# Optimization experiments

Hardware: AMD Instinct MI355X
Metric: run time of the kernel (lower is better)

Reference implementation:

```python
import jax, jax.numpy as jnp
import numpy as np

B, S, D = 4, 2048, 1024

def setup_inputs() -> dict:
    key = jax.random.key(0)
    kv, kk, kq, kw = jax.random.split(key, 4)
    scale = 1.0 / np.sqrt(D)
    v = jax.random.normal(kv, (B, S, D), dtype=jnp.float32)
    k = jax.random.normal(kk, (B, S, D), dtype=jnp.float32)
    q = jax.random.normal(kq, (B, S, D), dtype=jnp.float32)
    wi = jax.random.normal(kw, (D, D), dtype=jnp.float32) * scale
    mask = jnp.tril(jnp.ones((S, S), dtype=bool))[None, :, :]  # causal [1,S,S]
    return {"v": v, "k": k, "q": q, "wi": wi, "mask": mask}

def reference(v, k, q, wi, mask):
    # project q, k, v with the shared weight wi
    q = q @ wi
    k = k @ wi
    v = v @ wi
    # scaled dot-product scores [B,S,S]
    scores = jnp.einsum('bqd,bkd->bqk', q, k) / jnp.sqrt(jnp.asarray(q.shape[-1], q.dtype))
    scores = jnp.where(mask, scores, jnp.asarray(-1e10, scores.dtype))
    attn = jax.nn.softmax(scores, axis=-1)
    # residual: q + attn @ v
    return q + jnp.einsum('bqk,bkd->bqd', attn, v)
```

## Files before the change

### kernel.cpp

```cpp
#include <hip/hip_runtime.h>
#include <hip/hip_bf16.h>

typedef __hip_bfloat16 bf16;
typedef short bf16x8 __attribute__((ext_vector_type(8)));
typedef float f32x4 __attribute__((ext_vector_type(4)));

#define HT 16384

__device__ __forceinline__ void gload16(const void* g, void* l) {
    __builtin_amdgcn_global_load_lds(
        (const __attribute__((address_space(1))) void*)g,
        (__attribute__((address_space(3))) void*)l, 16, 0, 0);
}

__device__ __forceinline__ void stage_half(char* lds, const bf16* src, int ld,
                                           int rowbase, int k0, int slotIdx,
                                           int tid)
{
    char* dst = lds + (size_t)slotIdx * HT + tid * 16;
    const int sub = tid >> 3;
    const int cb  = ((tid & 7) ^ (sub & 7)) << 4;
    #pragma unroll
    for (int p = 0; p < 2; ++p) {
        const int row = p * 64 + sub;
        const char* g = (const char*)(src + (size_t)(rowbase + row) * ld + k0) + cb;
        gload16(g, dst + p * 8192);
    }
}

__device__ __forceinline__ bf16x8 ldsfrag(const char* lds, int slotIdx,
                                          int row, int ks, int cb0)
{
    return *(const bf16x8*)(lds + (size_t)slotIdx * HT
                            + row * 128 + (cb0 ^ (ks << 6)));
}

__device__ __forceinline__ float bf2f(short s) {
    union { float f; unsigned u; } c;
    c.u = ((unsigned)(unsigned short)s) << 16;
    return c.f;
}

__launch_bounds__(512, 2)
__global__ void proj_deep(const bf16* __restrict__ A, const bf16* __restrict__ B,
                          bf16* __restrict__ C)
{
    extern __shared__ char lds[];
    const int orig = blockIdx.y * 8 + blockIdx.x;
    const int wk2 = (orig & 7) * 96 + (orig >> 3);
    const int bi = wk2 >> 3, bj = wk2 & 7;
    const int brow = bi * 256, bcol = bj * 128;

    const int tid  = threadIdx.x;
    const int lane = tid & 63;
    const int w    = tid >> 6;
    const int wm   = w >> 1, wn = w & 1;
    const int fr   = lane & 15, fq = lane >> 4;
    const int cb0  = ((fr & 7) ^ fq) << 4;
    const int hA    = wm >> 1;
    const int rA    = (wm & 1) * 64;
    const int rB    = wn * 64;
    const int NT    = 16;

    f32x4 acc[4][4] = {};
    bf16x8 af[4][2], bv[4][2];

    stage_half(lds, A, 1024, brow,       0, 0, tid);
    stage_half(lds, A, 1024, brow + 128, 0, 1, tid);
    stage_half(lds, B, 1024, bcol,       0, 6, tid);
    stage_half(lds, A, 1024, brow,      64, 2, tid);
    stage_half(lds, A, 1024, brow + 128,64, 3, tid);
    stage_half(lds, B, 1024, bcol,     64, 7, tid);
    stage_half(lds, B, 1024, bcol,    128, 8, tid);
    asm volatile("s_waitcnt vmcnt(8)" ::: "memory");
    __builtin_amdgcn_s_barrier();

#define QUAD2(m0, n0)                                                         \
    _Pragma("unroll") for (int dm = 0; dm < 2; ++dm)                          \
    _Pragma("unroll") for (int dn = 0; dn < 2; ++dn)                          \
    _Pragma("unroll") for (int ks = 0; ks < 2; ++ks)                          \
        acc[(m0)+dm][(n0)+dn] = __builtin_amdgcn_mfma_f32_16x16x32_bf16(      \
            af[(m0)+dm][ks], bv[(n0)+dn][ks], acc[(m0)+dm][(n0)+dn], 0, 0, 0);

    for (int t = 0; t < NT; ++t) {
        const int ab  = t % 3;
        const int bb  = 6 + ab;
        const int ab2 = ((t + 2) % 3) * 2;
        const int kA  = min(t + 2, NT - 1) << 6;
        const int kB  = min(t + 3, NT - 1) << 6;
        const int slotA = ab * 2 + hA;

        #pragma unroll
        for (int m = 0; m < 2; ++m)
            #pragma unroll
            for (int ks = 0; ks < 2; ++ks)
                af[m][ks] = ldsfrag(lds, slotA, rA + m * 16 + fr, ks, cb0);
        #pragma unroll
        for (int n = 0; n < 2; ++n)
            #pragma unroll
            for (int ks = 0; ks < 2; ++ks)
                bv[n][ks] = ldsfrag(lds, bb, rB + n * 16 + fr, ks, cb0);
        stage_half(lds, A, 1024, brow, kA, ab2, tid);
        __builtin_amdgcn_s_barrier();
        __builtin_amdgcn_s_setprio(1);
        QUAD2(0, 0)
        __builtin_amdgcn_s_setprio(0);
        __builtin_amdgcn_s_barrier();

        #pragma unroll
        for (int n = 2; n < 4; ++n)
            #pragma unroll
            for (int ks = 0; ks < 2; ++ks)
                bv[n][ks] = ldsfrag(lds, bb, rB + n * 16 + fr, ks, cb0);
        stage_half(lds, A, 1024, brow + 128, kA, ab2 + 1, tid);
        __builtin_amdgcn_s_barrier();
        __builtin_amdgcn_s_setprio(1);
        QUAD2(0, 2)
        __builtin_amdgcn_s_setprio(0);
        __builtin_amdgcn_s_barrier();

        #pragma unroll
        for (int m = 2; m < 4; ++m)
            #pragma unroll
            for (int ks = 0; ks < 2; ++ks)
                af[m][ks] = ldsfrag(lds, slotA, rA + m * 16 + fr, ks, cb0);
        stage_half(lds, B, 1024, bcol, kB, bb, tid);
        __builtin_amdgcn_s_barrier();
        __builtin_amdgcn_s_setprio(1);
        QUAD2(2, 2)
        __builtin_amdgcn_s_setprio(0);
        __builtin_amdgcn_s_barrier();

        __builtin_amdgcn_s_setprio(1);
        QUAD2(2, 0)
        __builtin_amdgcn_s_setprio(0);
        asm volatile("s_waitcnt vmcnt(6)" ::: "memory");
        __builtin_amdgcn_s_barrier();
    }
#undef QUAD2

    #pragma unroll
    for (int mf = 0; mf < 4; ++mf) {
        const int r0 = brow + wm * 64 + mf * 16 + fq * 4;
        #pragma unroll
        for (int nf = 0; nf < 4; ++nf) {
            const int c = bcol + wn * 64 + nf * 16 + fr;
            #pragma unroll
            for (int j = 0; j < 4; ++j)
                C[(size_t)(r0 + j) * 1024 + c] = __float2bfloat16(acc[mf][nf][j]);
        }
    }
}

template<int MODE>
__device__ __forceinline__ void tile128(char* lds, const bf16* A, const bf16* B,
                                        bf16* Cb, float* Cf, const bf16* Res,
                                        int lda, int ldb, int ldcb,
                                        int brow, int bcol, int NT, float scale,
                                        int tid, int wm, int wn, int fr, int fq,
                                        int cb0)
{
    f32x4 acc[4][2] = {};
    bf16x8 af[4][2], bv[2][2];

    stage_half(lds, A, lda, brow, 0,  0, tid);
    stage_half(lds, B, ldb, bcol, 0,  3, tid);
    stage_half(lds, A, lda, brow, 64, 1, tid);
    stage_half(lds, B, ldb, bcol, 64, 4, tid);
    asm volatile("s_waitcnt vmcnt(4)" ::: "memory");
    __builtin_amdgcn_s_barrier();

    for (int t = 0; t < NT; ++t) {
        const int aslot = t % 3, bslot = 3 + (t & 1);
        const int k2 = min(t + 2, NT - 1) << 6;

        #pragma unroll
        for (int m = 0; m < 2; ++m)
            #pragma unroll
            for (int ks = 0; ks < 2; ++ks)
                af[m][ks] = ldsfrag(lds, aslot, wm * 64 + m * 16 + fr, ks, cb0);
        #pragma unroll
        for (int n = 0; n < 2; ++n)
            #pragma unroll
            for (int ks = 0; ks < 2; ++ks)
                bv[n][ks] = ldsfrag(lds, bslot, wn * 32 + n * 16 + fr, ks, cb0);
        stage_half(lds, A, lda, brow, k2, (t + 2) % 3, tid);
        __builtin_amdgcn_s_barrier();
        __builtin_amdgcn_s_setprio(1);
        #pragma unroll
        for (int m = 0; m < 2; ++m)
            #pragma unroll
            for (int n = 0; n < 2; ++n)
                #pragma unroll
                for (int ks = 0; ks < 2; ++ks)
                    acc[m][n] = __builtin_amdgcn_mfma_f32_16x16x32_bf16(
                        af[m][ks], bv[n][ks], acc[m][n], 0, 0, 0);
        __builtin_amdgcn_s_setprio(0);
        __builtin_amdgcn_s_barrier();

        #pragma unroll
        for (int m = 2; m < 4; ++m)
            #pragma unroll
            for (int ks = 0; ks < 2; ++ks)
                af[m][ks] = ldsfrag(lds, aslot, wm * 64 + m * 16 + fr, ks, cb0);
        stage_half(lds, B, ldb, bcol, k2, bslot, tid);
        __builtin_amdgcn_s_barrier();
        __builtin_amdgcn_s_setprio(1);
        #pragma unroll
        for (int m = 2; m < 4; ++m)
            #pragma unroll
            for (int n = 0; n < 2; ++n)
                #pragma unroll
                for (int ks = 0; ks < 2; ++ks)
                    acc[m][n] = __builtin_amdgcn_mfma_f32_16x16x32_bf16(
                        af[m][ks], bv[n][ks], acc[m][n], 0, 0, 0);
        __builtin_amdgcn_s_setprio(0);
        asm volatile("s_waitcnt vmcnt(4)" ::: "memory");
        __builtin_amdgcn_s_barrier();
    }

    #pragma unroll
    for (int mf = 0; mf < 4; ++mf) {
        const int r0 = brow + wm * 64 + mf * 16 + fq * 4;
        #pragma unroll
        for (int nf = 0; nf < 2; ++nf) {
            const int c = bcol + wn * 32 + nf * 16 + fr;
            #pragma unroll
            for (int j = 0; j < 4; ++j) {
                if (MODE == 1)
                    Cb[(size_t)(r0 + j) * ldcb + c] =
                        __float2bfloat16(acc[mf][nf][j] * scale);
                else
                    Cf[(size_t)(r0 + j) * ldcb + c] = acc[mf][nf][j] +
                        __bfloat162float(Res[(size_t)(r0 + j) * ldcb + c]);
            }
        }
    }
}

__launch_bounds__(512, 4)
__global__ void scores128(const bf16* __restrict__ qp, const bf16* __restrict__ kp,
                          bf16* __restrict__ P)
{
    extern __shared__ char lds[];
    const int j = blockIdx.x;
    int bi = (int)((__fsqrt_rn(8.0f * j + 1.0f) - 1.0f) * 0.5f);
    while ((bi + 1) * (bi + 2) / 2 <= j) ++bi;
    while (bi * (bi + 1) / 2 > j) --bi;
    const int bj = j - bi * (bi + 1) / 2;
    const int bz = blockIdx.z;

    const int tid  = threadIdx.x;
    const int lane = tid & 63;
    const int w    = tid >> 6;
    const int wm   = w >> 2, wn = w & 3;
    const int fr   = lane & 15, fq = lane >> 4;
    const int cb0  = ((fr & 7) ^ fq) << 4;

    tile128<1>(lds,
               qp + (size_t)bz * 2048 * 1024,
               kp + (size_t)bz * 2048 * 1024,
               P + (size_t)bz * 2048 * 2048, nullptr, nullptr,
               1024, 1024, 2048,
               bi * 128, bj * 128, 16, 0.03125f,
               tid, wm, wn, fr, fq, cb0);
}

__launch_bounds__(512, 4)
__global__ void pv128(const bf16* __restrict__ P, const bf16* __restrict__ V,
                      const bf16* __restrict__ R, float* __restrict__ C)
{
    extern __shared__ char lds[];
    const int pid = blockIdx.x, bj = blockIdx.y, bz = blockIdx.z;
    const bf16* Pb = P + (size_t)bz * 2048 * 2048;
    const bf16* Vb = V + (size_t)bz * 1024 * 2048;
    const bf16* Rb = R + (size_t)bz * 2048 * 1024;
    float* Cb = C + (size_t)bz * 2048 * 1024;

    const int tid  = threadIdx.x;
    const int lane = tid & 63;
    const int w    = tid >> 6;
    const int wm   = w >> 2, wn = w & 3;
    const int fr   = lane & 15, fq = lane >> 4;
    const int cb0  = ((fr & 7) ^ fq) << 4;
    const int bcol = bj * 128;

    tile128<2>(lds, Pb, Vb, nullptr, Cb, Rb, 2048, 2048, 1024,
               pid * 128, bcol, 2 * (pid + 1), 1.0f,
               tid, wm, wn, fr, fq, cb0);
    asm volatile("s_waitcnt vmcnt(0) lgkmcnt(0)" ::: "memory");
    __builtin_amdgcn_s_barrier();
    const int bi2 = 15 - pid;
    tile128<2>(lds, Pb, Vb, nullptr, Cb, Rb, 2048, 2048, 1024,
               bi2 * 128, bcol, 2 * (bi2 + 1), 1.0f,
               tid, wm, wn, fr, fq, cb0);
}

__global__ void convert_and_wi(const float* __restrict__ q,
                               const float* __restrict__ k,
                               const float* __restrict__ v,
                               const float* __restrict__ wi,
                               bf16* __restrict__ Xb, bf16* __restrict__ Wt)
{
    __shared__ float t[32][33];
    if (blockIdx.x < 1024) {
        const int n0 = (blockIdx.x & 31) * 32, k0 = (blockIdx.x >> 5) * 32;
        const int lx = threadIdx.x & 31, ly = threadIdx.x >> 5;
        for (int i = ly; i < 32; i += 8)
            t[i][lx] = wi[(size_t)(k0 + i) * 1024 + n0 + lx];
        __syncthreads();
        for (int i = ly; i < 32; i += 8)
            Wt[(size_t)(n0 + i) * 1024 + k0 + lx] = __float2bfloat16(t[lx][i]);
        return;
    }
    const int N8 = 8192 * 1024 / 8;
    const int total = 3 * N8;
    const int nconv = gridDim.x - 1024;
    for (int i = (blockIdx.x - 1024) * 256 + threadIdx.x; i < total;
         i += nconv * 256) {
        const int ti = i / N8, j = i - ti * N8;
        const float4* s = (ti == 0) ? (const float4*)q
                        : (ti == 1) ? (const float4*)k : (const float4*)v;
        float4 a = s[2 * j], bq = s[2 * j + 1];
        float vals[8] = {a.x, a.y, a.z, a.w, bq.x, bq.y, bq.z, bq.w};
        union { short h[8]; bf16x8 v8; } o;
        #pragma unroll
        for (int e = 0; e < 8; ++e) {
            bf16 hh = __float2bfloat16(vals[e]);
            o.h[e] = *(short*)&hh;
        }
        ((bf16x8*)Xb)[i] = o.v8;
    }
}

__global__ void transpose_vp(const bf16* __restrict__ vp, bf16* __restrict__ vpT)
{
    __shared__ bf16 t[32][33];
    const int b = blockIdx.z;
    const int d0 = blockIdx.x * 32, s0 = blockIdx.y * 32;
    const bf16* src = vp + (size_t)b * 2048 * 1024;
    bf16* dst = vpT + (size_t)b * 1024 * 2048;
    const int lx = threadIdx.x & 31, ly = threadIdx.x >> 5;
    for (int i = ly; i < 32; i += 8)
        t[i][lx] = src[(size_t)(s0 + i) * 1024 + d0 + lx];
    __syncthreads();
    for (int i = ly; i < 32; i += 8)
        dst[(size_t)(d0 + i) * 2048 + s0 + lx] = t[lx][i];
}

__launch_bounds__(256)
__global__ void softmax_rows(bf16* __restrict__ P)
{
    const int wid = threadIdx.x >> 6, lane = threadIdx.x & 63;
    const int r = blockIdx.x * 4 + wid, b = blockIdx.y;
    bf16* row = P + ((size_t)b * 2048 + r) * 2048;
    const int nv  = r + 1;
    const int rup = (r & ~127) + 128;

    float vals[4][8];
    float m = -1e30f;
    #pragma unroll
    for (int c = 0; c < 4; ++c) {
        const int k0 = c * 512 + lane * 8;
        if (k0 < rup) {
            bf16x8 x = *(const bf16x8*)(row + k0);
            #pragma unroll
            for (int j = 0; j < 8; ++j) {
                float f = (k0 + j < nv) ? bf2f(x[j]) : -1e30f;
                vals[c][j] = f;
                m = fmaxf(m, f);
            }
        } else {
            #pragma unroll
            for (int j = 0; j < 8; ++j) vals[c][j] = -1e30f;
        }
    }
    #pragma unroll
    for (int o = 32; o; o >>= 1) m = fmaxf(m, __shfl_xor(m, o));

    float sum = 0.f;
    #pragma unroll
    for (int c = 0; c < 4; ++c)
        #pragma unroll
        for (int j = 0; j < 8; ++j) {
            float e = __expf(vals[c][j] - m);
            vals[c][j] = e;
            sum += e;
        }
    #pragma unroll
    for (int o = 32; o; o >>= 1) sum += __shfl_xor(sum, o);
    const float inv = 1.0f / sum;

    #pragma unroll
    for (int c = 0; c < 4; ++c) {
        const int k0 = c * 512 + lane * 8;
        if (k0 < rup) {
            union { short h[8]; bf16x8 v8; } o;
            #pragma unroll
            for (int j = 0; j < 8; ++j) {
                bf16 hh = __float2bfloat16(vals[c][j] * inv);
                o.h[j] = *(short*)&hh;
            }
            *(bf16x8*)(row + k0) = o.v8;
        }
    }
}

extern "C" void kernel_launch(void* const* d_in, const int* in_sizes, int n_in,
                              void* d_out, int out_size, void* d_ws, size_t ws_size,
                              hipStream_t stream)
{
    const float* v  = (const float*)d_in[0];
    const float* k  = (const float*)d_in[1];
    const float* q  = (const float*)d_in[2];
    const float* wi = (const float*)d_in[3];
    float* out = (float*)d_out;

    char* ws = (char*)d_ws;
    const size_t WT_OFF   = 0;
    const size_t PROJ_OFF = WT_OFF + (2u << 20);
    const size_t VPT_OFF  = PROJ_OFF + (size_t)24576 * 1024 * 2;
    const size_t XB_OFF   = VPT_OFF + (size_t)4 * 1024 * 2048 * 2;

    bf16* Wt   = (bf16*)(ws + WT_OFF);
    bf16* proj = (bf16*)(ws + PROJ_OFF);
    bf16* vpT  = (bf16*)(ws + VPT_OFF);
    bf16* Xb   = (bf16*)(ws + XB_OFF);
    bf16* P    = Xb;

    bf16* qp_b = proj;
    bf16* kp_b = proj + (size_t)8192 * 1024;
    bf16* vp_b = proj + (size_t)16384 * 1024;

    (void)hipFuncSetAttribute((const void*)proj_deep,
            hipFuncAttributeMaxDynamicSharedMemorySize, 147456);
    (void)hipFuncSetAttribute((const void*)scores128,
            hipFuncAttributeMaxDynamicSharedMemorySize, 81920);
    (void)hipFuncSetAttribute((const void*)pv128,
            hipFuncAttributeMaxDynamicSharedMemorySize, 81920);

    convert_and_wi<<<3072, 256, 0, stream>>>(q, k, v, wi, Xb, Wt);

    proj_deep<<<dim3(8, 96), 512, 147456, stream>>>(Xb, Wt, proj);

    transpose_vp<<<dim3(32, 64, 4), 256, 0, stream>>>(vp_b, vpT);

    scores128<<<dim3(136, 1, 4), 512, 81920, stream>>>(qp_b, kp_b, P);

    softmax_rows<<<dim3(512, 4), 256, 0, stream>>>(P);

    pv128<<<dim3(8, 8, 4), 512, 81920, stream>>>(P, vpT, qp_b, out);
}
```

Baseline: 180.6 us.

## Use 4-wave 64x64 warp tiles for scores/PV and simplify projection pipeline

The scores and PV kernels move from 512 threads with 32x64 per-wave tiles to 256 threads where each wave computes a 64x64 tile, staging tiles through a new quarter-row loader. The PV kernel is re-gridded to one 128x128 tile per block (512 blocks) rather than each block processing a pair of complementary causal tiles. The projection kernel switches to a two-phase K loop with double-buffered B and less LDS. The aim is more register-level reuse per MFMA and simpler scheduling, at the cost of fewer waves per block, higher register pressure, and a less balanced PV causal workload per block.

```diff
diff --git a/kernel.cpp b/kernel.cpp
--- a/kernel.cpp
+++ b/kernel.cpp
@@ -28,6 +28,21 @@
     }
 }
 
+__device__ __forceinline__ void stage_q(char* lds, const bf16* src, int ld,
+                                        int rowbase, int k0, int slotIdx,
+                                        int tid)
+{
+    char* dst = lds + (size_t)slotIdx * HT + tid * 16;
+    #pragma unroll
+    for (int p = 0; p < 4; ++p) {
+        const int s = p * 256 + tid;
+        const int row = s >> 3;
+        const int cb = ((s & 7) ^ (row & 7)) << 4;
+        const char* g = (const char*)(src + (size_t)(rowbase + row) * ld + k0) + cb;
+        gload16(g, dst + p * 4096);
+    }
+}
+
 __device__ __forceinline__ bf16x8 ldsfrag(const char* lds, int slotIdx,
                                           int row, int ks, int cb0)
 {
@@ -42,8 +57,8 @@
 }
 
 __launch_bounds__(512, 2)
-__global__ void proj_deep(const bf16* __restrict__ A, const bf16* __restrict__ B,
-                          bf16* __restrict__ C)
+__global__ void proj_2ph(const bf16* __restrict__ A, const bf16* __restrict__ B,
+                         bf16* __restrict__ C)
 {
     extern __shared__ char lds[];
     const int orig = blockIdx.y * 8 + blockIdx.x;
@@ -57,10 +72,10 @@
     const int wm   = w >> 1, wn = w & 1;
     const int fr   = lane & 15, fq = lane >> 4;
     const int cb0  = ((fr & 7) ^ fq) << 4;
-    const int hA    = wm >> 1;
-    const int rA    = (wm & 1) * 64;
-    const int rB    = wn * 64;
-    const int NT    = 16;
+    const int hA   = wm >> 1;
+    const int rA   = (wm & 1) * 64;
+    const int rB   = wn * 64;
+    const int NT   = 16;
 
     f32x4 acc[4][4] = {};
     bf16x8 af[4][2], bv[4][2];
@@ -71,73 +86,49 @@
     stage_half(lds, A, 1024, brow,      64, 2, tid);
     stage_half(lds, A, 1024, brow + 128,64, 3, tid);
     stage_half(lds, B, 1024, bcol,     64, 7, tid);
-    stage_half(lds, B, 1024, bcol,    128, 8, tid);
-    asm volatile("s_waitcnt vmcnt(8)" ::: "memory");
+    asm volatile("s_waitcnt vmcnt(6)" ::: "memory");
     __builtin_amdgcn_s_barrier();
 
-#define QUAD2(m0, n0)                                                         \
-    _Pragma("unroll") for (int dm = 0; dm < 2; ++dm)                          \
+#define MF8(n0)                                                               \
+    _Pragma("unroll") for (int m = 0; m < 4; ++m)                             \
     _Pragma("unroll") for (int dn = 0; dn < 2; ++dn)                          \
     _Pragma("unroll") for (int ks = 0; ks < 2; ++ks)                          \
-        acc[(m0)+dm][(n0)+dn] = __builtin_amdgcn_mfma_f32_16x16x32_bf16(      \
-            af[(m0)+dm][ks], bv[(n0)+dn][ks], acc[(m0)+dm][(n0)+dn], 0, 0, 0);
+        acc[m][(n0)+dn] = __builtin_amdgcn_mfma_f32_16x16x32_bf16(            \
+            af[m][ks], bv[(n0)+dn][ks], acc[m][(n0)+dn], 0, 0, 0);
 
     for (int t = 0; t < NT; ++t) {
-        const int ab  = t % 3;
-        const int bb  = 6 + ab;
-        const int ab2 = ((t + 2) % 3) * 2;
-        const int kA  = min(t + 2, NT - 1) << 6;
-        const int kB  = min(t + 3, NT - 1) << 6;
-        const int slotA = ab * 2 + hA;
-
-        #pragma unroll
-        for (int m = 0; m < 2; ++m)
+        const int aslot = (t % 3) * 2 + hA;
+        const int bslot = 6 + (t & 1);
+        const int a2    = ((t + 2) % 3) * 2;
+        const int k2    = min(t + 2, NT - 1) << 6;
+
+        #pragma unroll
+        for (int m = 0; m < 4; ++m)
             #pragma unroll
             for (int ks = 0; ks < 2; ++ks)
-                af[m][ks] = ldsfrag(lds, slotA, rA + m * 16 + fr, ks, cb0);
-        #pragma unroll
-        for (int n = 0; n < 2; ++n)
+                af[m][ks] = ldsfrag(lds, aslot, rA + m * 16 + fr, ks, cb0);
+        #pragma unroll
+        for (int n = 0; n < 4; ++n)
             #pragma unroll
             for (int ks = 0; ks < 2; ++ks)
-                bv[n][ks] = ldsfrag(lds, bb, rB + n * 16 + fr, ks, cb0);
-        stage_half(lds, A, 1024, brow, kA, ab2, tid);
+                bv[n][ks] = ldsfrag(lds, bslot, rB + n * 16 + fr, ks, cb0);
+        stage_half(lds, A, 1024, brow,       k2, a2,     tid);
+        stage_half(lds, A, 1024, brow + 128, k2, a2 + 1, tid);
         __builtin_amdgcn_s_barrier();
         __builtin_amdgcn_s_setprio(1);
-        QUAD2(0, 0)
+        MF8(0)
         __builtin_amdgcn_s_setprio(0);
         __builtin_amdgcn_s_barrier();
 
-        #pragma unroll
-        for (int n = 2; n < 4; ++n)
-            #pragma unroll
-            for (int ks = 0; ks < 2; ++ks)
-                bv[n][ks] = ldsfrag(lds, bb, rB + n * 16 + fr, ks, cb0);
-        stage_half(lds, A, 1024, brow + 128, kA, ab2 + 1, tid);
+        stage_half(lds, B, 1024, bcol, k2, bslot, tid);
         __builtin_amdgcn_s_barrier();
         __builtin_amdgcn_s_setprio(1);
-        QUAD2(0, 2)
-        __builtin_amdgcn_s_setprio(0);
-        __builtin_amdgcn_s_barrier();
-
-        #pragma unroll
-        for (int m = 2; m < 4; ++m)
-            #pragma unroll
-            for (int ks = 0; ks < 2; ++ks)
-                af[m][ks] = ldsfrag(lds, slotA, rA + m * 16 + fr, ks, cb0);
-        stage_half(lds, B, 1024, bcol, kB, bb, tid);
-        __builtin_amdgcn_s_barrier();
-        __builtin_amdgcn_s_setprio(1);
-        QUAD2(2, 2)
-        __builtin_amdgcn_s_setprio(0);
-        __builtin_amdgcn_s_barrier();
-
-        __builtin_amdgcn_s_setprio(1);
-        QUAD2(2, 0)
+        MF8(2)
         __builtin_amdgcn_s_setprio(0);
         asm volatile("s_waitcnt vmcnt(6)" ::: "memory");
         __builtin_amdgcn_s_barrier();
     }
-#undef QUAD2
+#undef MF8
 
     #pragma unroll
     for (int mf = 0; mf < 4; ++mf) {
@@ -153,21 +144,26 @@
 }
 
 template<int MODE>
-__device__ __forceinline__ void tile128(char* lds, const bf16* A, const bf16* B,
-                                        bf16* Cb, float* Cf, const bf16* Res,
-                                        int lda, int ldb, int ldcb,
-                                        int brow, int bcol, int NT, float scale,
-                                        int tid, int wm, int wn, int fr, int fq,
-                                        int cb0)
-{
-    f32x4 acc[4][2] = {};
-    bf16x8 af[4][2], bv[2][2];
-
-    stage_half(lds, A, lda, brow, 0,  0, tid);
-    stage_half(lds, B, ldb, bcol, 0,  3, tid);
-    stage_half(lds, A, lda, brow, 64, 1, tid);
-    stage_half(lds, B, ldb, bcol, 64, 4, tid);
-    asm volatile("s_waitcnt vmcnt(4)" ::: "memory");
+__device__ __forceinline__ void tile128v2(char* lds, const bf16* A, const bf16* B,
+                                          bf16* Cb, float* Cf, const bf16* Res,
+                                          int lda, int ldb, int ldcb,
+                                          int brow, int bcol, int NT, float scale,
+                                          int tid)
+{
+    const int lane = tid & 63;
+    const int w    = tid >> 6;
+    const int wm   = w >> 1, wn = w & 1;
+    const int fr   = lane & 15, fq = lane >> 4;
+    const int cb0  = ((fr & 7) ^ fq) << 4;
+
+    f32x4 acc[4][4] = {};
+    bf16x8 af[4][2], bv[4][2];
+
+    stage_q(lds, A, lda, brow, 0,  0, tid);
+    stage_q(lds, B, ldb, bcol, 0,  3, tid);
+    stage_q(lds, A, lda, brow, 64, 1, tid);
+    stage_q(lds, B, ldb, bcol, 64, 4, tid);
+    asm volatile("s_waitcnt vmcnt(8)" ::: "memory");
     __builtin_amdgcn_s_barrier();
 
     for (int t = 0; t < NT; ++t) {
@@ -175,20 +171,20 @@
         const int k2 = min(t + 2, NT - 1) << 6;
 
         #pragma unroll
-        for (int m = 0; m < 2; ++m)
+        for (int m = 0; m < 4; ++m)
             #pragma unroll
             for (int ks = 0; ks < 2; ++ks)
                 af[m][ks] = ldsfrag(lds, aslot, wm * 64 + m * 16 + fr, ks, cb0);
         #pragma unroll
-        for (int n = 0; n < 2; ++n)
+        for (int n = 0; n < 4; ++n)
             #pragma unroll
             for (int ks = 0; ks < 2; ++ks)
-                bv[n][ks] = ldsfrag(lds, bslot, wn * 32 + n * 16 + fr, ks, cb0);
-        stage_half(lds, A, lda, brow, k2, (t + 2) % 3, tid);
+                bv[n][ks] = ldsfrag(lds, bslot, wn * 64 + n * 16 + fr, ks, cb0);
+        stage_q(lds, A, lda, brow, k2, (t + 2) % 3, tid);
         __builtin_amdgcn_s_barrier();
         __builtin_amdgcn_s_setprio(1);
         #pragma unroll
-        for (int m = 0; m < 2; ++m)
+        for (int m = 0; m < 4; ++m)
             #pragma unroll
             for (int n = 0; n < 2; ++n)
                 #pragma unroll
@@ -198,24 +194,19 @@
         __builtin_amdgcn_s_setprio(0);
         __builtin_amdgcn_s_barrier();
 
-        #pragma unroll
-        for (int m = 2; m < 4; ++m)
-            #pragma unroll
-            for (int ks = 0; ks < 2; ++ks)
-                af[m][ks] = ldsfrag(lds, aslot, wm * 64 + m * 16 + fr, ks, cb0);
-        stage_half(lds, B, ldb, bcol, k2, bslot, tid);
+        stage_q(lds, B, ldb, bcol, k2, bslot, tid);
         __builtin_amdgcn_s_barrier();
         __builtin_amdgcn_s_setprio(1);
         #pragma unroll
-        for (int m = 2; m < 4; ++m)
-            #pragma unroll
-            for (int n = 0; n < 2; ++n)
+        for (int m = 0; m < 4; ++m)
+            #pragma unroll
+            for (int n = 2; n < 4; ++n)
                 #pragma unroll
                 for (int ks = 0; ks < 2; ++ks)
                     acc[m][n] = __builtin_amdgcn_mfma_f32_16x16x32_bf16(
                         af[m][ks], bv[n][ks], acc[m][n], 0, 0, 0);
         __builtin_amdgcn_s_setprio(0);
-        asm volatile("s_waitcnt vmcnt(4)" ::: "memory");
+        asm volatile("s_waitcnt vmcnt(8)" ::: "memory");
         __builtin_amdgcn_s_barrier();
     }
 
@@ -223,8 +214,8 @@
     for (int mf = 0; mf < 4; ++mf) {
         const int r0 = brow + wm * 64 + mf * 16 + fq * 4;
         #pragma unroll
-        for (int nf = 0; nf < 2; ++nf) {
-            const int c = bcol + wn * 32 + nf * 16 + fr;
+        for (int nf = 0; nf < 4; ++nf) {
+            const int c = bcol + wn * 64 + nf * 16 + fr;
             #pragma unroll
             for (int j = 0; j < 4; ++j) {
                 if (MODE == 1)
@@ -238,7 +229,7 @@
     }
 }
 
-__launch_bounds__(512, 4)
+__launch_bounds__(256, 2)
 __global__ void scores128(const bf16* __restrict__ qp, const bf16* __restrict__ kp,
                           bf16* __restrict__ P)
 {
@@ -250,50 +241,34 @@
     const int bj = j - bi * (bi + 1) / 2;
     const int bz = blockIdx.z;
 
-    const int tid  = threadIdx.x;
-    const int lane = tid & 63;
-    const int w    = tid >> 6;
-    const int wm   = w >> 2, wn = w & 3;
-    const int fr   = lane & 15, fq = lane >> 4;
-    const int cb0  = ((fr & 7) ^ fq) << 4;
-
-    tile128<1>(lds,
-               qp + (size_t)bz * 2048 * 1024,
-               kp + (size_t)bz * 2048 * 1024,
-               P + (size_t)bz * 2048 * 2048, nullptr, nullptr,
-               1024, 1024, 2048,
-               bi * 128, bj * 128, 16, 0.03125f,
-               tid, wm, wn, fr, fq, cb0);
-}
-
-__launch_bounds__(512, 4)
+    tile128v2<1>(lds,
+                 qp + (size_t)bz * 2048 * 1024,
+                 kp + (size_t)bz * 2048 * 1024,
+                 P + (size_t)bz * 2048 * 2048, nullptr, nullptr,
+                 1024, 1024, 2048,
+                 bi * 128, bj * 128, 16, 0.03125f, threadIdx.x);
+}
+
+__launch_bounds__(256, 2)
 __global__ void pv128(const bf16* __restrict__ P, const bf16* __restrict__ V,
                       const bf16* __restrict__ R, float* __restrict__ C)
 {
     extern __shared__ char lds[];
-    const int pid = blockIdx.x, bj = blockIdx.y, bz = blockIdx.z;
-    const bf16* Pb = P + (size_t)bz * 2048 * 2048;
-    const bf16* Vb = V + (size_t)bz * 1024 * 2048;
-    const bf16* Rb = R + (size_t)bz * 2048 * 1024;
-    float* Cb = C + (size_t)bz * 2048 * 1024;
-
-    const int tid  = threadIdx.x;
-    const int lane = tid & 63;
-    const int w    = tid >> 6;
-    const int wm   = w >> 2, wn = w & 3;
-    const int fr   = lane & 15, fq = lane >> 4;
-    const int cb0  = ((fr & 7) ^ fq) << 4;
-    const int bcol = bj * 128;
-
-    tile128<2>(lds, Pb, Vb, nullptr, Cb, Rb, 2048, 2048, 1024,
-               pid * 128, bcol, 2 * (pid + 1), 1.0f,
-               tid, wm, wn, fr, fq, cb0);
-    asm volatile("s_waitcnt vmcnt(0) lgkmcnt(0)" ::: "memory");
-    __builtin_amdgcn_s_barrier();
-    const int bi2 = 15 - pid;
-    tile128<2>(lds, Pb, Vb, nullptr, Cb, Rb, 2048, 2048, 1024,
-               bi2 * 128, bcol, 2 * (bi2 + 1), 1.0f,
-               tid, wm, wn, fr, fq, cb0);
+    const int x  = blockIdx.x;
+    const int u  = x & 255;
+    const int bs = u & 7;
+    const int bj = (u >> 3) & 7;
+    const int bz = u >> 6;
+    const int bi = (x >> 8) ? (15 - bs) : bs;
+
+    tile128v2<2>(lds,
+                 P + (size_t)bz * 2048 * 2048,
+                 V + (size_t)bz * 1024 * 2048,
+                 nullptr,
+                 C + (size_t)bz * 2048 * 1024,
+                 R + (size_t)bz * 2048 * 1024,
+                 2048, 2048, 1024,
+                 bi * 128, bj * 128, 2 * (bi + 1), 1.0f, threadIdx.x);
 }
 
 __global__ void convert_and_wi(const float* __restrict__ q,
@@ -432,8 +407,8 @@
     bf16* kp_b = proj + (size_t)8192 * 1024;
     bf16* vp_b = proj + (size_t)16384 * 1024;
 
-    (void)hipFuncSetAttribute((const void*)proj_deep,
-            hipFuncAttributeMaxDynamicSharedMemorySize, 147456);
+    (void)hipFuncSetAttribute((const void*)proj_2ph,
+            hipFuncAttributeMaxDynamicSharedMemorySize, 131072);
     (void)hipFuncSetAttribute((const void*)scores128,
             hipFuncAttributeMaxDynamicSharedMemorySize, 81920);
     (void)hipFuncSetAttribute((const void*)pv128,
@@ -441,13 +416,13 @@
 
     convert_and_wi<<<3072, 256, 0, stream>>>(q, k, v, wi, Xb, Wt);
 
-    proj_deep<<<dim3(8, 96), 512, 147456, stream>>>(Xb, Wt, proj);
+    proj_2ph<<<dim3(8, 96), 512, 131072, stream>>>(Xb, Wt, proj);
 
     transpose_vp<<<dim3(32, 64, 4), 256, 0, stream>>>(vp_b, vpT);
 
-    scores128<<<dim3(136, 1, 4), 512, 81920, stream>>>(qp_b, kp_b, P);
+    scores128<<<dim3(136, 1, 4), 256, 81920, stream>>>(qp_b, kp_b, P);
 
     softmax_rows<<<dim3(512, 4), 256, 0, stream>>>(P);
 
-    pv128<<<dim3(8, 8, 4), 512, 81920, stream>>>(P, vpT, qp_b, out);
-}
+    pv128<<<dim3(512), 256, 81920, stream>>>(P, vpT, qp_b, out);
+}
```

New measurement: 179.1 us. No clear change (-0.9%).
